# Kernel optimization log

Measured on AMD Instinct MI355X. Metric: run time of the kernel, lower is better.

Reference implementation:

```python
import jax, jax.numpy as jnp
import numpy as np


def reference(x, y, max_disp):
    # x, y: [B, C, H, W] left/right feature maps (stride-3 features)
    # Builds cost[b, :C, i, h, w]  = x[b, :, h, w]      for w >= i else 0
    #        cost[b, C:, i, h, w] = y[b, :, h, w - i]  for w >= i else 0
    # i.e. the vectorized form of the original Python loop over disparities.
    D = max_disp // 3
    B, C, H, W = x.shape
    d = jnp.arange(D)
    w = jnp.arange(W)
    mask = (w[None, :] >= d[:, None]).astype(x.dtype)          # [D, W]
    m = mask[None, None, :, None, :]                            # [1,1,D,1,W]
    cost_x = x[:, :, None, :, :] * m                            # [B,C,D,H,W]
    idx = jnp.clip(w[None, :] - d[:, None], 0, W - 1)           # [D, W]
    y_shift = y[:, :, :, idx]                                   # [B,C,H,D,W]
    cost_y = jnp.transpose(y_shift, (0, 1, 3, 2, 4)) * m        # [B,C,D,H,W]
    return jnp.concatenate([cost_x, cost_y], axis=1)            # [B,2C,D,H,W]


def setup_inputs() -> dict:
    key = jax.random.key(0)
    k1, k2 = jax.random.split(key)
    B, C, H, W = 1, 32, 96, 192
    x = jax.random.normal(k1, (B, C, H, W), dtype=jnp.float32)
    y = jax.random.normal(k2, (B, C, H, W), dtype=jnp.float32)
    return {"x": x, "y": y, "max_disp": 192}
```

## Files before the change

kernel.cpp:

```cpp
#include <hip/hip_runtime.h>

constexpr int C     = 32;
constexpr int D     = 64;
constexpr int H     = 96;
constexpr int W     = 192;
constexpr int W4    = W / 4;
constexpr int HB    = 6;
constexpr int HITER = 16;

typedef float f4  __attribute__((ext_vector_type(4)));
typedef float f4u __attribute__((ext_vector_type(4), aligned(4)));

__global__ __launch_bounds__(256) void fusion_kernel(const float* __restrict__ x,
                                                     const float* __restrict__ y,
                                                     float* __restrict__ out) {
    const int tid = blockIdx.x * blockDim.x + threadIdx.x;
    const int w4  = tid % W4;
    int rest      = tid / W4;
    const int hb  = rest % HB;
    rest         /= HB;
    const int d   = rest % D;
    const int ch  = rest / D;
    const int w   = w4 * 4;
    const int h0  = hb * HITER;

    const int outoff = (ch * D + d) * (H * W) + h0 * W + w;

    const bool m0 = (w + 0) < d;
    const bool m1 = (w + 1) < d;
    const bool m2 = (w + 2) < d;
    const bool m3 = (w + 3) < d;

    f4 v[HITER];

    if (ch < C) {
        const float* xr = x + ch * (H * W) + h0 * W + w;
        #pragma unroll
        for (int i = 0; i < HITER; ++i)
            v[i] = *(const f4*)(xr + i * W);
    } else {
        const int off0 = (ch - C) * (H * W) + h0 * W + w - d;
        if (off0 >= 0) {
            v[0] = *(const f4u*)(y + off0);
        } else {
            v[0].x = y[max(off0 + 0, 0)];
            v[0].y = y[max(off0 + 1, 0)];
            v[0].z = y[max(off0 + 2, 0)];
            v[0].w = y[max(off0 + 3, 0)];
        }
        #pragma unroll
        for (int i = 1; i < HITER; ++i)
            v[i] = *(const f4u*)(y + off0 + i * W);
    }

    #pragma unroll
    for (int i = 0; i < HITER; ++i) {
        f4 s = v[i];
        if (m0) s.x = 0.f;
        if (m1) s.y = 0.f;
        if (m2) s.z = 0.f;
        if (m3) s.w = 0.f;
        *(f4*)(out + outoff + i * W) = s;
    }
}

extern "C" void kernel_launch(void* const* d_in, const int* in_sizes, int n_in,
                              void* d_out, int out_size, void* d_ws, size_t ws_size,
                              hipStream_t stream) {
    const float* x = (const float*)d_in[0];
    const float* y = (const float*)d_in[1];
    float* out     = (float*)d_out;

    constexpr int total = 2 * C * D * HB * W4;
    constexpr int block = 256;
    constexpr int grid  = total / block;
    fusion_kernel<<<grid, block, 0, stream>>>(x, y, out);
}
```

Measured before the change: 311.4 us.

## Remap thread work so each store instruction writes contiguous output across planes

Threads are re-indexed so that thread tid writes output float4 slots tid + i*NTH for 16 strided planes. Consecutive threads now cover contiguous HW spans within a plane. Each thread loads 8 x channels and 8 shifted y channels, all sharing the same disparity mask. This aims to make every wave-level store a fully contiguous run and to simplify index math. Loads now jump across channels rather than rows, which may reduce locality within a thread.

```diff
diff --git a/kernel.cpp b/kernel.cpp
--- a/kernel.cpp
+++ b/kernel.cpp
@@ -1,12 +1,12 @@
 #include <hip/hip_runtime.h>
 
-constexpr int C     = 32;
-constexpr int D     = 64;
-constexpr int H     = 96;
-constexpr int W     = 192;
-constexpr int W4    = W / 4;
-constexpr int HB    = 6;
-constexpr int HITER = 16;
+constexpr int C      = 32;
+constexpr int D      = 64;
+constexpr int H      = 96;
+constexpr int W      = 192;
+constexpr int HW     = H * W;
+constexpr int PLANE4 = HW / 4;
+constexpr int NTH    = 2 * C * D * PLANE4 / 16;
 
 typedef float f4  __attribute__((ext_vector_type(4)));
 typedef float f4u __attribute__((ext_vector_type(4), aligned(4)));
@@ -14,53 +14,47 @@
 __global__ __launch_bounds__(256) void fusion_kernel(const float* __restrict__ x,
                                                      const float* __restrict__ y,
                                                      float* __restrict__ out) {
-    const int tid = blockIdx.x * blockDim.x + threadIdx.x;
-    const int w4  = tid % W4;
-    int rest      = tid / W4;
-    const int hb  = rest % HB;
-    rest         /= HB;
-    const int d   = rest % D;
-    const int ch  = rest / D;
-    const int w   = w4 * 4;
-    const int h0  = hb * HITER;
-
-    const int outoff = (ch * D + d) * (H * W) + h0 * W + w;
+    const int tid    = blockIdx.x * blockDim.x + threadIdx.x;
+    const int plane0 = tid / PLANE4;
+    const int rem    = tid - plane0 * PLANE4;
+    const int d      = plane0 & 63;
+    const int ch0    = plane0 >> 6;
+    const int w      = (rem % 48) * 4;
 
     const bool m0 = (w + 0) < d;
     const bool m1 = (w + 1) < d;
     const bool m2 = (w + 2) < d;
     const bool m3 = (w + 3) < d;
 
-    f4 v[HITER];
+    const int xoff0 = ch0 * HW + rem * 4;
+    const int yoff0 = xoff0 - d;
 
-    if (ch < C) {
-        const float* xr = x + ch * (H * W) + h0 * W + w;
-        #pragma unroll
-        for (int i = 0; i < HITER; ++i)
-            v[i] = *(const f4*)(xr + i * W);
-    } else {
-        const int off0 = (ch - C) * (H * W) + h0 * W + w - d;
-        if (off0 >= 0) {
-            v[0] = *(const f4u*)(y + off0);
-        } else {
-            v[0].x = y[max(off0 + 0, 0)];
-            v[0].y = y[max(off0 + 1, 0)];
-            v[0].z = y[max(off0 + 2, 0)];
-            v[0].w = y[max(off0 + 3, 0)];
-        }
-        #pragma unroll
-        for (int i = 1; i < HITER; ++i)
-            v[i] = *(const f4u*)(y + off0 + i * W);
-    }
+    f4 v[16];
 
     #pragma unroll
-    for (int i = 0; i < HITER; ++i) {
+    for (int i = 0; i < 8; ++i)
+        v[i] = *(const f4*)(x + xoff0 + i * (4 * HW));
+
+    if (yoff0 >= 0) {
+        v[8] = *(const f4u*)(y + yoff0);
+    } else {
+        v[8].x = y[max(yoff0 + 0, 0)];
+        v[8].y = y[max(yoff0 + 1, 0)];
+        v[8].z = y[max(yoff0 + 2, 0)];
+        v[8].w = y[max(yoff0 + 3, 0)];
+    }
+    #pragma unroll
+    for (int i = 1; i < 8; ++i)
+        v[8 + i] = *(const f4u*)(y + yoff0 + i * (4 * HW));
+
+    #pragma unroll
+    for (int i = 0; i < 16; ++i) {
         f4 s = v[i];
         if (m0) s.x = 0.f;
         if (m1) s.y = 0.f;
         if (m2) s.z = 0.f;
         if (m3) s.w = 0.f;
-        *(f4*)(out + outoff + i * W) = s;
+        *(f4*)(out + (tid + i * NTH) * 4) = s;
     }
 }
 
@@ -71,8 +65,7 @@
     const float* y = (const float*)d_in[1];
     float* out     = (float*)d_out;
 
-    constexpr int total = 2 * C * D * HB * W4;
     constexpr int block = 256;
-    constexpr int grid  = total / block;
+    constexpr int grid  = NTH / block;
     fusion_kernel<<<grid, block, 0, stream>>>(x, y, out);
 }
```

New measurement: 301.8 us. 1.03x faster.
